# Kernel optimization log

Measured on AMD Instinct MI355X. Metric: run time of the kernel, lower is better.

The kernel has to match this reference:

```python
import jax, jax.numpy as jnp
import numpy as np

B, C, H, W = 4, 512, 64, 64
KEY_DIM, VALUE_DIM = 512, 512


def setup_inputs() -> dict:
    key = jax.random.key(0)
    k1, k2, k3, k4 = jax.random.split(key, 4)
    s = 1.0 / np.sqrt(C).astype(np.float32)
    x = jax.random.normal(k1, (B, C, H, W), jnp.float32)
    # torch nn.Linear weights have shape (out_features, in_features)
    Wk = jax.random.normal(k2, (KEY_DIM, C), jnp.float32) * s
    Wq = jax.random.normal(k3, (KEY_DIM, C), jnp.float32) * s
    Wv = jax.random.normal(k4, (VALUE_DIM, C), jnp.float32) * s
    return {"x": x, "Wk": Wk, "Wq": Wq, "Wv": Wv}


def reference(x, Wk, Wq, Wv):
    b, c, h, w = x.shape
    kd = Wk.shape[0]
    n = h * w
    # (b,c,h,w) -> (b, n, c) tokens, matching transpose+flatten in the original
    xt = x.transpose(0, 2, 3, 1).reshape(b, n, c)
    q = xt @ Wq.T  # (b, n, kd)
    k = xt @ Wk.T  # (b, n, kd)
    v = xt @ Wv.T  # (b, n, vd)
    scaling = np.sqrt(float(kd)).astype(np.float32)
    scores = jax.nn.softmax(jnp.einsum('bnd,bmd->bnm', q, k) / scaling, axis=-1)
    # original: output[j] = sum_i values[i] * scores[j, i]  ==  scores @ V
    out = jnp.einsum('bnm,bmv->bnv', scores, v)  # (b, n, vd)
    # original scores_out: sum over dim=0 (query index) of the (n, n) score matrix
    scores_out = scores.sum(axis=1).reshape(b, 1, h, w)
    out = out.reshape(b, h, w, -1).transpose(0, 3, 1, 2)  # (b, vd, h, w)
    return out, scores_out
```

## Files before the change

### kernel.cpp

```cpp
#include <hip/hip_runtime.h>


typedef short bf16x8 __attribute__((ext_vector_type(8)));
typedef float f32x4 __attribute__((ext_vector_type(4)));

#define NTOK 4096
#define DDIM 512
#define NB   4

__device__ __forceinline__ unsigned short f32_bf16(float f) {
  union { float f; unsigned u; } v; v.f = f;
  unsigned r = v.u + 0x7FFFu + ((v.u >> 16) & 1u);
  return (unsigned short)(r >> 16);
}

__device__ __forceinline__ float bf16_f32(short s) {
  union { unsigned u; float f; } v;
  v.u = ((unsigned)(unsigned short)s) << 16;
  return v.f;
}

__device__ __forceinline__ void gload_lds16(const unsigned short* g,
                                            unsigned short* l) {
  __builtin_amdgcn_global_load_lds(
      (__attribute__((address_space(1))) void*)(g),
      (__attribute__((address_space(3))) void*)(l), 16, 0, 0);
}

__global__ __launch_bounds__(256, 4) void qkv_proj(
    const float* __restrict__ x,
    const float* __restrict__ Wq,
    const float* __restrict__ Wk,
    const float* __restrict__ Wv,
    unsigned short* __restrict__ Qt,
    unsigned short* __restrict__ Kf,
    unsigned short* __restrict__ Vt)
{
  const int nt0 = blockIdx.x * 64;
  const int d0  = blockIdx.y * 64;
  const int b   = blockIdx.z;
  const int tid = threadIdx.x;
  const int wave = tid >> 6;
  const int lane = tid & 63;
  const int l15  = lane & 15;
  const int quad = lane >> 4;

  __shared__ __align__(16) unsigned short Xt[64 * 40];
  __shared__ __align__(16) unsigned short Wl[3][64 * 40];

  f32x4 aq[4], ak[4], av[4];
#pragma unroll
  for (int i = 0; i < 4; ++i) {
    aq[i] = (f32x4){0.f,0.f,0.f,0.f};
    ak[i] = (f32x4){0.f,0.f,0.f,0.f};
    av[i] = (f32x4){0.f,0.f,0.f,0.f};
  }

  const float* xb = x + (size_t)b * DDIM * NTOK + nt0;
  const int xn  = tid & 63;
  const int xc8 = tid >> 6;
  const int wc8 = tid & 3;
  const int wdd = tid >> 2;

  for (int cc = 0; cc < DDIM; cc += 32) {
    __syncthreads();
    {
      bf16x8 t;
#pragma unroll
      for (int j = 0; j < 8; ++j)
        t[j] = (short)f32_bf16(xb[(size_t)(cc + xc8 * 8 + j) * NTOK + xn]);
      *(bf16x8*)(&Xt[xn * 40 + xc8 * 8]) = t;
    }
    {
      const float* wsrc[3] = {Wq, Wk, Wv};
#pragma unroll
      for (int m = 0; m < 3; ++m) {
        const float* src = wsrc[m] + (size_t)(d0 + wdd) * DDIM + cc + wc8 * 8;
        bf16x8 t;
#pragma unroll
        for (int j = 0; j < 8; ++j) t[j] = (short)f32_bf16(src[j]);
        *(bf16x8*)(&Wl[m][wdd * 40 + wc8 * 8]) = t;
      }
    }
    __syncthreads();

    bf16x8 xa  = *(const bf16x8*)(&Xt[(wave * 16 + l15) * 40 + quad * 8]);
    bf16x8 wva = *(const bf16x8*)(&Wl[2][(wave * 16 + l15) * 40 + quad * 8]);
#pragma unroll
    for (int nt = 0; nt < 4; ++nt) {
      bf16x8 wqf = *(const bf16x8*)(&Wl[0][(nt * 16 + l15) * 40 + quad * 8]);
      bf16x8 wkf = *(const bf16x8*)(&Wl[1][(nt * 16 + l15) * 40 + quad * 8]);
      bf16x8 xbf = *(const bf16x8*)(&Xt[(nt * 16 + l15) * 40 + quad * 8]);
      aq[nt] = __builtin_amdgcn_mfma_f32_16x16x32_bf16(xa,  wqf, aq[nt], 0, 0, 0);
      ak[nt] = __builtin_amdgcn_mfma_f32_16x16x32_bf16(xa,  wkf, ak[nt], 0, 0, 0);
      av[nt] = __builtin_amdgcn_mfma_f32_16x16x32_bf16(wva, xbf, av[nt], 0, 0, 0);
    }
  }

#pragma unroll
  for (int nt = 0; nt < 4; ++nt) {
#pragma unroll
    for (int r = 0; r < 4; ++r) {
      const int tokq = nt0 + wave * 16 + quad * 4 + r;
      const int dq   = d0 + nt * 16 + l15;
      Qt[((size_t)b * NTOK + tokq) * DDIM + dq] = f32_bf16(aq[nt][r]);
      {
        const int kblk  = (nt0 >> 4) + wave;
        const int dc    = (d0 >> 5) + (nt >> 1);
        const int laneK = ((nt & 1) * 2 + (l15 >> 3)) * 16 + quad * 4 + r;
        Kf[((size_t)(b * 256 + kblk) * 16 + dc) * 512 + laneK * 8 + (l15 & 7)] =
            f32_bf16(ak[nt][r]);
      }
      const int dblk  = (d0 >> 4) + wave;
      const int ic    = (nt0 >> 5) + (nt >> 1);
      const int laneV = ((nt & 1) * 2 + (l15 >> 3)) * 16 + quad * 4 + r;
      Vt[(size_t)b * DDIM * NTOK +
         ((size_t)(dblk * 128 + ic) * 64 + laneV) * 8 + (l15 & 7)] =
          f32_bf16(av[nt][r]);
    }
  }
}

#define SCALE 0.044194173824159216f

__global__ __launch_bounds__(256, 2) void attn_lsum_p(
    const unsigned short* __restrict__ Qt,
    const unsigned short* __restrict__ Kf,
    unsigned short* __restrict__ Pt,
    float* __restrict__ lsum_g)
{
  const int qb = blockIdx.x;
  const int kp = blockIdx.y;
  const int b  = blockIdx.z;
  const int tid  = threadIdx.x;
  const int wave = tid >> 6;
  const int lane = tid & 63;
  const int l15  = lane & 15;
  const int quad = lane >> 4;
  const int q0   = qb * 128 + wave * 32;

  __shared__ __align__(16) unsigned short Klds[2][16384];

  bf16x8 qf[2][16];
#pragma unroll
  for (int qt = 0; qt < 2; ++qt) {
    const unsigned short* qp =
        Qt + ((size_t)b * NTOK + q0 + qt * 16 + l15) * DDIM + quad * 8;
#pragma unroll
    for (int dc = 0; dc < 16; ++dc) qf[qt][dc] = *(const bf16x8*)(qp + dc * 32);
  }

  unsigned short* Pq = Pt + (size_t)b * NTOK * NTOK +
                       (size_t)(qb * 2 + (wave >> 1)) * 262144;
  const int ntb = (wave & 1) * 2;

  float ls[2][4] = {{0.f,0.f,0.f,0.f},{0.f,0.f,0.f,0.f}};

  const unsigned short* Ksrc0 = Kf + ((size_t)(b * 256 + kp * 64) * 16) * 512;

#define KSTAGE(KC_, B_)                                                        \
  do {                                                                         \
    const unsigned short* ks_ = Ksrc0 + (size_t)(KC_)*16384;                   \
    _Pragma("unroll") for (int c_ = 0; c_ < 8; ++c_) {                         \
      const int ch_ = c_ * 4 + wave;                                           \
      gload_lds16(ks_ + ch_ * 512 + lane * 8, &Klds[B_][ch_ * 512]);           \
    }                                                                          \
  } while (0)

  KSTAGE(0, 0);
  __syncthreads();

  for (int kc2 = 0; kc2 < 32; ++kc2) {
    const int cb = kc2 & 1;
    if (kc2 < 31) KSTAGE(kc2 + 1, cb ^ 1);

#pragma unroll
    for (int kt = 0; kt < 2; ++kt) {
      const int kabs = kp * 64 + kc2 * 2 + kt;
      f32x4 s0 = (f32x4){0.f,0.f,0.f,0.f};
      f32x4 s1 = (f32x4){0.f,0.f,0.f,0.f};
#pragma unroll
      for (int dc = 0; dc < 16; ++dc) {
        const bf16x8 kbf =
            *(const bf16x8*)(&Klds[cb][(kt * 16 + dc) * 512 + lane * 8]);
        s0 = __builtin_amdgcn_mfma_f32_16x16x32_bf16(qf[0][dc], kbf, s0, 0, 0, 0);
        s1 = __builtin_amdgcn_mfma_f32_16x16x32_bf16(qf[1][dc], kbf, s1, 0, 0, 0);
      }
      const int ic    = kabs >> 1;
      const int lt_hi = ((kabs & 1) * 2 + (l15 >> 3)) * 16;
      const int jj    = l15 & 7;
#pragma unroll
      for (int r = 0; r < 4; ++r) {
        const float e0 = __expf(s0[r] * SCALE);
        const float e1 = __expf(s1[r] * SCALE);
        ls[0][r] += e0;
        ls[1][r] += e1;
        Pq[((size_t)(ic * 4 + ntb) * 64 + lt_hi + quad * 4 + r) * 8 + jj] =
            f32_bf16(e0);
        Pq[((size_t)(ic * 4 + ntb + 1) * 64 + lt_hi + quad * 4 + r) * 8 + jj] =
            f32_bf16(e1);
      }
    }
    __syncthreads();
  }
#undef KSTAGE

#pragma unroll
  for (int qt = 0; qt < 2; ++qt)
#pragma unroll
    for (int r = 0; r < 4; ++r) {
      float v = ls[qt][r];
      v += __shfl_xor(v, 1);
      v += __shfl_xor(v, 2);
      v += __shfl_xor(v, 4);
      v += __shfl_xor(v, 8);
      if (l15 == 0)
        unsafeAtomicAdd(&lsum_g[(size_t)b * NTOK + q0 + qt * 16 + quad * 4 + r], v);
    }
}

__global__ __launch_bounds__(256, 4) void attn_pv(
    const unsigned short* __restrict__ Pt,
    const unsigned short* __restrict__ Vt,
    const float* __restrict__ lsum_g,
    float* __restrict__ out)
{
  const int g     = blockIdx.x;
  const int xcd   = g & 7;
  const int slot  = g >> 3;
  const int combo = (xcd << 1) | (slot >> 6);
  const int q0b   = slot & 63;
  const int dpart = combo & 3;
  const int b     = combo >> 2;
  const int tid  = threadIdx.x;
  const int wave = tid >> 6;
  const int lane = tid & 63;
  const int l15  = lane & 15;
  const int quad = lane >> 4;

  const int dblk0 = dpart * 8 + wave * 2;
  const unsigned short* Pq =
      Pt + (size_t)b * NTOK * NTOK + (size_t)q0b * 262144;
  const unsigned short* Vb =
      Vt + (size_t)b * DDIM * NTOK + lane * 8;

  __shared__ __align__(16) unsigned short Plds[2][8192];

  float rlv[4];
#pragma unroll
  for (int nt = 0; nt < 4; ++nt)
    rlv[nt] = 1.0f / lsum_g[(size_t)b * NTOK + q0b * 64 + nt * 16 + l15];

  f32x4 o[2][4];
#pragma unroll
  for (int i = 0; i < 2; ++i)
#pragma unroll
    for (int j = 0; j < 4; ++j) o[i][j] = (f32x4){0.f,0.f,0.f,0.f};

  bf16x8 vA[2], vB[2];

#define LOADVN(D_, IC_)                                                        \
  do {                                                                         \
    _Pragma("unroll") for (int mt = 0; mt < 2; ++mt)                           \
      D_[mt] = *(const bf16x8*)(Vb + (size_t)(dblk0 + mt) * 65536 +            \
                                (size_t)(IC_)*512);                            \
  } while (0)

#define PSTAGE(S_, B_)                                                         \
  do {                                                                         \
    const unsigned short* ps_ = Pq + (size_t)(S_)*8192;                        \
    _Pragma("unroll") for (int c_ = 0; c_ < 4; ++c_) {                         \
      const int ch_ = c_ * 4 + wave;                                           \
      gload_lds16(ps_ + ch_ * 512 + lane * 8, &Plds[B_][ch_ * 512]);           \
    }                                                                          \
  } while (0)

  LOADVN(vA, 0);
  LOADVN(vB, 1);
  PSTAGE(0, 0);
  __syncthreads();

  for (int s = 0; s < 32; ++s) {
    const int cb = s & 1;
    if (s < 31) PSTAGE(s + 1, cb ^ 1);
#pragma unroll
    for (int i = 0; i < 4; ++i) {
      const int ic = s * 4 + i;
      bf16x8 pb[4];
#pragma unroll
      for (int nt = 0; nt < 4; ++nt)
        pb[nt] = *(const bf16x8*)(&Plds[cb][i * 2048 + nt * 512 + lane * 8]);
      if ((i & 1) == 0) {
#pragma unroll
        for (int mt = 0; mt < 2; ++mt)
#pragma unroll
          for (int nt = 0; nt < 4; ++nt)
            o[mt][nt] = __builtin_amdgcn_mfma_f32_16x16x32_bf16(
                vA[mt], pb[nt], o[mt][nt], 0, 0, 0);
        if (ic + 2 < 128) LOADVN(vA, ic + 2);
      } else {
#pragma unroll
        for (int mt = 0; mt < 2; ++mt)
#pragma unroll
          for (int nt = 0; nt < 4; ++nt)
            o[mt][nt] = __builtin_amdgcn_mfma_f32_16x16x32_bf16(
                vB[mt], pb[nt], o[mt][nt], 0, 0, 0);
        if (ic + 2 < 128) LOADVN(vB, ic + 2);
      }
    }
    __syncthreads();
  }
#undef LOADVN
#undef PSTAGE

  float* ob = out + ((size_t)b * DDIM + dpart * 128 + wave * 32) * NTOK + q0b * 64;
#pragma unroll
  for (int mt = 0; mt < 2; ++mt)
#pragma unroll
    for (int nt = 0; nt < 4; ++nt)
#pragma unroll
      for (int r = 0; r < 4; ++r)
        ob[(size_t)(mt * 16 + quad * 4 + r) * NTOK + nt * 16 + l15] =
            o[mt][nt][r] * rlv[nt];
}

__global__ __launch_bounds__(256, 4) void colsum_k(
    const unsigned short* __restrict__ Pt,
    const float* __restrict__ lsum_g,
    float* __restrict__ scores_out)
{
  const int ic = blockIdx.x;
  const int b  = blockIdx.y;
  const int tid = threadIdx.x;
  const int wave = tid >> 6;
  const int lane = tid & 63;
  const int l15  = lane & 15;
  const int quad = lane >> 4;

  __shared__ float red[4][32];

  const unsigned short* Pb = Pt + (size_t)b * NTOK * NTOK + (size_t)ic * 2048 + lane * 8;
  const float* lb = lsum_g + (size_t)b * NTOK;

  float acc[8];
#pragma unroll
  for (int j = 0; j < 8; ++j) acc[j] = 0.f;

  for (int q0b = wave; q0b < 64; q0b += 4) {
    const unsigned short* src = Pb + (size_t)q0b * 262144;
#pragma unroll
    for (int nt = 0; nt < 4; ++nt) {
      const bf16x8 p = *(const bf16x8*)(src + (size_t)nt * 512);
      const float rl = 1.0f / lb[q0b * 64 + nt * 16 + l15];
#pragma unroll
      for (int j = 0; j < 8; ++j) acc[j] = fmaf(bf16_f32(p[j]), rl, acc[j]);
    }
  }
#pragma unroll
  for (int j = 0; j < 8; ++j) {
    float v = acc[j];
    v += __shfl_xor(v, 1);
    v += __shfl_xor(v, 2);
    v += __shfl_xor(v, 4);
    v += __shfl_xor(v, 8);
    acc[j] = v;
  }
  if (l15 == 0) {
#pragma unroll
    for (int j = 0; j < 8; ++j) red[wave][quad * 8 + j] = acc[j];
  }
  __syncthreads();
  if (tid < 32)
    scores_out[(size_t)b * NTOK + ic * 32 + tid] =
        red[0][tid] + red[1][tid] + red[2][tid] + red[3][tid];
}

extern "C" void kernel_launch(void* const* d_in, const int* in_sizes, int n_in,
                              void* d_out, int out_size, void* d_ws, size_t ws_size,
                              hipStream_t stream) {
  const float* x  = (const float*)d_in[0];
  const float* Wk = (const float*)d_in[1];
  const float* Wq = (const float*)d_in[2];
  const float* Wv = (const float*)d_in[3];

  float* out = (float*)d_out;
  float* scores_out = out + (size_t)NB * DDIM * NTOK;

  const size_t mat_elems = (size_t)NB * NTOK * DDIM;
  unsigned short* Qt = (unsigned short*)d_ws;
  unsigned short* Kf = Qt + mat_elems;
  unsigned short* Vt = Kf + mat_elems;
  float* lbuf = (float*)(Vt + mat_elems);
  unsigned short* Pt = (unsigned short*)(lbuf + (size_t)NB * NTOK);

  hipMemsetAsync(lbuf, 0, (size_t)NB * NTOK * sizeof(float), stream);

  dim3 g1(NTOK / 64, DDIM / 64, NB);
  qkv_proj<<<g1, 256, 0, stream>>>(x, Wq, Wk, Wv, Qt, Kf, Vt);

  dim3 g2(NTOK / 128, 4, NB);
  attn_lsum_p<<<g2, 256, 0, stream>>>(Qt, Kf, Pt, lbuf);

  attn_pv<<<dim3(1024), 256, 0, stream>>>(Pt, Vt, lbuf, out);

  dim3 g4(128, NB);
  colsum_k<<<g4, 256, 0, stream>>>(Pt, lbuf, scores_out);
}
```

Baseline: 346.2 us.

## Read K directly from global memory with XCD-aware block remapping

Drops the double-buffered LDS staging of K and the per-iteration block barriers in the score kernel, so each wave reads its K fragments straight from global memory. The 3D grid becomes a 1D grid of 512 blocks, remapped so that blocks on the same XCD share the same batch and key partition, which should keep K resident in that XCD's L2. This removes the LDS traffic and barrier stalls, but global load latency now sits directly in front of the MFMA chain with no explicit prefetch, and performance now depends on L2 hit rates.

After: 545.7 us. 57.6% more time.

```diff
diff --git a/kernel.cpp b/kernel.cpp
--- a/kernel.cpp
+++ b/kernel.cpp
@@ -129,9 +129,13 @@
     unsigned short* __restrict__ Pt,
     float* __restrict__ lsum_g)
 {
-  const int qb = blockIdx.x;
-  const int kp = blockIdx.y;
-  const int b  = blockIdx.z;
+  const int g     = blockIdx.x;
+  const int xcd   = g & 7;
+  const int slot  = g >> 3;
+  const int combo = (xcd << 1) | (slot >> 5);
+  const int qb    = slot & 31;
+  const int kp    = combo & 3;
+  const int b     = combo >> 2;
   const int tid  = threadIdx.x;
   const int wave = tid >> 6;
   const int lane = tid & 63;
@@ -139,8 +143,6 @@
   const int quad = lane >> 4;
   const int q0   = qb * 128 + wave * 32;
 
-  __shared__ __align__(16) unsigned short Klds[2][16384];
-
   bf16x8 qf[2][16];
 #pragma unroll
   for (int qt = 0; qt < 2; ++qt) {
@@ -156,54 +158,34 @@
 
   float ls[2][4] = {{0.f,0.f,0.f,0.f},{0.f,0.f,0.f,0.f}};
 
-  const unsigned short* Ksrc0 = Kf + ((size_t)(b * 256 + kp * 64) * 16) * 512;
-
-#define KSTAGE(KC_, B_)                                                        \
-  do {                                                                         \
-    const unsigned short* ks_ = Ksrc0 + (size_t)(KC_)*16384;                   \
-    _Pragma("unroll") for (int c_ = 0; c_ < 8; ++c_) {                         \
-      const int ch_ = c_ * 4 + wave;                                           \
-      gload_lds16(ks_ + ch_ * 512 + lane * 8, &Klds[B_][ch_ * 512]);           \
-    }                                                                          \
-  } while (0)
-
-  KSTAGE(0, 0);
-  __syncthreads();
-
-  for (int kc2 = 0; kc2 < 32; ++kc2) {
-    const int cb = kc2 & 1;
-    if (kc2 < 31) KSTAGE(kc2 + 1, cb ^ 1);
-
-#pragma unroll
-    for (int kt = 0; kt < 2; ++kt) {
-      const int kabs = kp * 64 + kc2 * 2 + kt;
-      f32x4 s0 = (f32x4){0.f,0.f,0.f,0.f};
-      f32x4 s1 = (f32x4){0.f,0.f,0.f,0.f};
-#pragma unroll
-      for (int dc = 0; dc < 16; ++dc) {
-        const bf16x8 kbf =
-            *(const bf16x8*)(&Klds[cb][(kt * 16 + dc) * 512 + lane * 8]);
-        s0 = __builtin_amdgcn_mfma_f32_16x16x32_bf16(qf[0][dc], kbf, s0, 0, 0, 0);
-        s1 = __builtin_amdgcn_mfma_f32_16x16x32_bf16(qf[1][dc], kbf, s1, 0, 0, 0);
-      }
-      const int ic    = kabs >> 1;
-      const int lt_hi = ((kabs & 1) * 2 + (l15 >> 3)) * 16;
-      const int jj    = l15 & 7;
-#pragma unroll
-      for (int r = 0; r < 4; ++r) {
-        const float e0 = __expf(s0[r] * SCALE);
-        const float e1 = __expf(s1[r] * SCALE);
-        ls[0][r] += e0;
-        ls[1][r] += e1;
-        Pq[((size_t)(ic * 4 + ntb) * 64 + lt_hi + quad * 4 + r) * 8 + jj] =
-            f32_bf16(e0);
-        Pq[((size_t)(ic * 4 + ntb + 1) * 64 + lt_hi + quad * 4 + r) * 8 + jj] =
-            f32_bf16(e1);
-      }
-    }
-    __syncthreads();
-  }
-#undef KSTAGE
+  const unsigned short* Kbase =
+      Kf + ((size_t)(b * 256 + kp * 64) * 16) * 512 + lane * 8;
+
+  for (int kb = 0; kb < 64; ++kb) {
+    const int kabs = kp * 64 + kb;
+    f32x4 s0 = (f32x4){0.f,0.f,0.f,0.f};
+    f32x4 s1 = (f32x4){0.f,0.f,0.f,0.f};
+#pragma unroll
+    for (int dc = 0; dc < 16; ++dc) {
+      const bf16x8 kbf = *(const bf16x8*)(Kbase + ((size_t)kb * 16 + dc) * 512);
+      s0 = __builtin_amdgcn_mfma_f32_16x16x32_bf16(qf[0][dc], kbf, s0, 0, 0, 0);
+      s1 = __builtin_amdgcn_mfma_f32_16x16x32_bf16(qf[1][dc], kbf, s1, 0, 0, 0);
+    }
+    const int ic    = kabs >> 1;
+    const int lt_hi = ((kabs & 1) * 2 + (l15 >> 3)) * 16;
+    const int jj    = l15 & 7;
+#pragma unroll
+    for (int r = 0; r < 4; ++r) {
+      const float e0 = __expf(s0[r] * SCALE);
+      const float e1 = __expf(s1[r] * SCALE);
+      ls[0][r] += e0;
+      ls[1][r] += e1;
+      Pq[((size_t)(ic * 4 + ntb) * 64 + lt_hi + quad * 4 + r) * 8 + jj] =
+          f32_bf16(e0);
+      Pq[((size_t)(ic * 4 + ntb + 1) * 64 + lt_hi + quad * 4 + r) * 8 + jj] =
+          f32_bf16(e1);
+    }
+  }
 
 #pragma unroll
   for (int qt = 0; qt < 2; ++qt)
@@ -398,8 +380,7 @@
   dim3 g1(NTOK / 64, DDIM / 64, NB);
   qkv_proj<<<g1, 256, 0, stream>>>(x, Wq, Wk, Wv, Qt, Kf, Vt);
 
-  dim3 g2(NTOK / 128, 4, NB);
-  attn_lsum_p<<<g2, 256, 0, stream>>>(Qt, Kf, Pt, lbuf);
+  attn_lsum_p<<<dim3(512), 256, 0, stream>>>(Qt, Kf, Pt, lbuf);
 
   attn_pv<<<dim3(1024), 256, 0, stream>>>(Pt, Vt, lbuf, out);
 
```

## Fuse score column-sum into PV kernel using LDS-resident P tiles

Applied to the files above, without the earlier changes.

The column sums of the normalized score matrix are now computed inside attn_pv from the P tiles already staged in LDS. Each dpart block covers one quarter of the key chunks, and per-query-block partial sums are written to a workspace buffer. A small reduce kernel then sums the 64 partials per token. This removes a second full read of the 4096x4096 bf16 P matrix per batch. In exchange it adds ALU and shuffle work inside the MFMA loop and needs extra workspace.

Result: slower. 355.2 us (+2.6%).

```diff
diff --git a/kernel.cpp b/kernel.cpp
--- a/kernel.cpp
+++ b/kernel.cpp
@@ -223,7 +223,8 @@
     const unsigned short* __restrict__ Pt,
     const unsigned short* __restrict__ Vt,
     const float* __restrict__ lsum_g,
-    float* __restrict__ out)
+    float* __restrict__ out,
+    float* __restrict__ scpart)
 {
   const int g     = blockIdx.x;
   const int xcd   = g & 7;
@@ -243,6 +244,7 @@
       Pt + (size_t)b * NTOK * NTOK + (size_t)q0b * 262144;
   const unsigned short* Vb =
       Vt + (size_t)b * DDIM * NTOK + lane * 8;
+  float* scp = scpart + ((size_t)(b * 64 + q0b)) * NTOK;
 
   __shared__ __align__(16) unsigned short Plds[2][8192];
 
@@ -283,6 +285,7 @@
   for (int s = 0; s < 32; ++s) {
     const int cb = s & 1;
     if (s < 31) PSTAGE(s + 1, cb ^ 1);
+    const bool own = ((s >> 3) == dpart);
 #pragma unroll
     for (int i = 0; i < 4; ++i) {
       const int ic = s * 4 + i;
@@ -307,6 +310,21 @@
                 vB[mt], pb[nt], o[mt][nt], 0, 0, 0);
         if (ic + 2 < 128) LOADVN(vB, ic + 2);
       }
+      if (own) {
+#pragma unroll
+        for (int jo = 0; jo < 2; ++jo) {
+          const int j = wave * 2 + jo;
+          float c = 0.f;
+#pragma unroll
+          for (int nt = 0; nt < 4; ++nt)
+            c = fmaf(bf16_f32(pb[nt][j]), rlv[nt], c);
+          c += __shfl_xor(c, 1);
+          c += __shfl_xor(c, 2);
+          c += __shfl_xor(c, 4);
+          c += __shfl_xor(c, 8);
+          if (l15 == 0) scp[ic * 32 + quad * 8 + j] = c;
+        }
+      }
     }
     __syncthreads();
   }
@@ -324,55 +342,17 @@
             o[mt][nt][r] * rlv[nt];
 }
 
-__global__ __launch_bounds__(256, 4) void colsum_k(
-    const unsigned short* __restrict__ Pt,
-    const float* __restrict__ lsum_g,
+__global__ __launch_bounds__(256, 8) void colsum_reduce(
+    const float* __restrict__ scpart,
     float* __restrict__ scores_out)
 {
-  const int ic = blockIdx.x;
-  const int b  = blockIdx.y;
-  const int tid = threadIdx.x;
-  const int wave = tid >> 6;
-  const int lane = tid & 63;
-  const int l15  = lane & 15;
-  const int quad = lane >> 4;
-
-  __shared__ float red[4][32];
-
-  const unsigned short* Pb = Pt + (size_t)b * NTOK * NTOK + (size_t)ic * 2048 + lane * 8;
-  const float* lb = lsum_g + (size_t)b * NTOK;
-
-  float acc[8];
-#pragma unroll
-  for (int j = 0; j < 8; ++j) acc[j] = 0.f;
-
-  for (int q0b = wave; q0b < 64; q0b += 4) {
-    const unsigned short* src = Pb + (size_t)q0b * 262144;
-#pragma unroll
-    for (int nt = 0; nt < 4; ++nt) {
-      const bf16x8 p = *(const bf16x8*)(src + (size_t)nt * 512);
-      const float rl = 1.0f / lb[q0b * 64 + nt * 16 + l15];
-#pragma unroll
-      for (int j = 0; j < 8; ++j) acc[j] = fmaf(bf16_f32(p[j]), rl, acc[j]);
-    }
-  }
-#pragma unroll
-  for (int j = 0; j < 8; ++j) {
-    float v = acc[j];
-    v += __shfl_xor(v, 1);
-    v += __shfl_xor(v, 2);
-    v += __shfl_xor(v, 4);
-    v += __shfl_xor(v, 8);
-    acc[j] = v;
-  }
-  if (l15 == 0) {
-#pragma unroll
-    for (int j = 0; j < 8; ++j) red[wave][quad * 8 + j] = acc[j];
-  }
-  __syncthreads();
-  if (tid < 32)
-    scores_out[(size_t)b * NTOK + ic * 32 + tid] =
-        red[0][tid] + red[1][tid] + red[2][tid] + red[3][tid];
+  const int b = blockIdx.y;
+  const int i = blockIdx.x * 256 + threadIdx.x;
+  const float* src = scpart + (size_t)b * 64 * NTOK + i;
+  float s = 0.f;
+#pragma unroll
+  for (int q = 0; q < 64; ++q) s += src[(size_t)q * NTOK];
+  scores_out[(size_t)b * NTOK + i] = s;
 }
 
 extern "C" void kernel_launch(void* const* d_in, const int* in_sizes, int n_in,
@@ -392,6 +372,7 @@
   unsigned short* Vt = Kf + mat_elems;
   float* lbuf = (float*)(Vt + mat_elems);
   unsigned short* Pt = (unsigned short*)(lbuf + (size_t)NB * NTOK);
+  float* scpart = (float*)(Pt + (size_t)NB * NTOK * NTOK);
 
   hipMemsetAsync(lbuf, 0, (size_t)NB * NTOK * sizeof(float), stream);
 
@@ -401,8 +382,7 @@
   dim3 g2(NTOK / 128, 4, NB);
   attn_lsum_p<<<g2, 256, 0, stream>>>(Qt, Kf, Pt, lbuf);
 
-  attn_pv<<<dim3(1024), 256, 0, stream>>>(Pt, Vt, lbuf, out);
-
-  dim3 g4(128, NB);
-  colsum_k<<<g4, 256, 0, stream>>>(Pt, lbuf, scores_out);
-}
+  attn_pv<<<dim3(1024), 256, 0, stream>>>(Pt, Vt, lbuf, out, scpart);
+
+  colsum_reduce<<<dim3(NTOK / 256, NB), 256, 0, stream>>>(scpart, scores_out);
+}
```
